# Performance work log

Hardware: AMD Instinct MI355X
Metric: run time of the kernel (lower is better)

## Reference

```python
import jax, jax.numpy as jnp
import numpy as np

EPS = 1e-5
H, I, E = 1024, 2048, 8


def _swiglu(x, wg, wu, wd):
    # x: [T,H], wg/wu: [H,I], wd: [I,H]
    return (jax.nn.silu(x @ wg) * (x @ wu)) @ wd


def setup_inputs() -> dict:
    key = jax.random.key(0)
    ks = jax.random.split(key, 12)
    B, S = 2, 2048
    s_h = 1.0 / np.sqrt(H)
    s_i = 1.0 / np.sqrt(I)
    return {
        "x": jax.random.normal(ks[0], (B, S, H), jnp.float32),
        "temporal_context": jax.random.normal(ks[1], (B, S, H), jnp.float32),
        "tp_w": jax.random.normal(ks[2], (H, H), jnp.float32) * s_h,
        "tp_b": jnp.zeros((H,), jnp.float32),
        "gate_w": jax.random.normal(ks[3], (H, E), jnp.float32) * 0.01,
        "eg": jax.random.normal(ks[4], (E, H, I), jnp.float32) * s_h,
        "eu": jax.random.normal(ks[5], (E, H, I), jnp.float32) * s_h,
        "ed": jax.random.normal(ks[6], (E, I, H), jnp.float32) * s_i,
        "sg": jax.random.normal(ks[7], (H, I), jnp.float32) * s_h,
        "su": jax.random.normal(ks[8], (H, I), jnp.float32) * s_h,
        "sd": jax.random.normal(ks[9], (I, H), jnp.float32) * s_i,
        "top_k": 2,
    }


def reference(x, temporal_context, tp_w, tp_b, gate_w, eg, eu, ed, sg, su, sd, top_k):
    B, S, Hd = x.shape
    xf = x.reshape(-1, Hd)                      # [T,H] tokens
    tc = temporal_context.reshape(-1, Hd)
    # Router: add temporal projection, softmax gate, top-k renormalized
    xr = xf + tc @ tp_w + tp_b
    probs = jax.nn.softmax(xr @ gate_w, axis=-1)            # [T,E]
    topk_p, topk_i = jax.lax.top_k(probs, top_k)            # [T,K]
    topk_p = topk_p / (topk_p.sum(-1, keepdims=True) + EPS)
    # Dense combine weights: combine[t,e] = sum_k topk_p[t,k] * 1[topk_i[t,k]==e]
    combine = jnp.einsum("tke,tk->te", jax.nn.one_hot(topk_i, E, dtype=x.dtype), topk_p)
    # Expert SwiGLU (grouped GEMM over all experts)
    h = jax.nn.silu(jnp.einsum("th,ehi->tei", xf, eg)) * jnp.einsum("th,ehi->tei", xf, eu)
    eout = jnp.einsum("tei,eih->teh", h, ed)                # [T,E,H]
    out = jnp.einsum("te,teh->th", combine, eout)
    # Shared expert applied to every token
    out = out + _swiglu(xf, sg, su, sd)
    return out.reshape(B, S, Hd)
```

## Files before the change

kernel.cpp:

```cpp
#include <hip/hip_runtime.h>
#include <hip/hip_bf16.h>
#include <stdint.h>

#define HDIM 1024
#define IDIM 2048
#define NEXP 8
#define NEXP1 9
#define TTOK 4096
#define REPS 1e-5f

typedef __bf16 bf16_t;
typedef __bf16 bf16x8 __attribute__((ext_vector_type(8)));
typedef __bf16 bf16x4 __attribute__((ext_vector_type(4)));
typedef float f32x4 __attribute__((ext_vector_type(4)));

__device__ __forceinline__ void gl_lds16(const bf16_t* g, bf16_t* l) {
    __builtin_amdgcn_global_load_lds(
        (const __attribute__((address_space(1))) void*)g,
        (__attribute__((address_space(3))) void*)l, 16, 0, 0);
}

__global__ __launch_bounds__(256) void k_convert(const float* __restrict__ src,
                                                 bf16_t* __restrict__ dst) {
    size_t i = ((size_t)blockIdx.x * 256 + threadIdx.x) * 4;
    float4 v = *(const float4*)(src + i);
    bf16x4 o = {(__bf16)v.x, (__bf16)v.y, (__bf16)v.z, (__bf16)v.w};
    *(bf16x4*)(dst + i) = o;
}

__global__ __launch_bounds__(256) void k_tr(const float* __restrict__ src,
                                            bf16_t* __restrict__ dst, int R, int C) {
    __shared__ __align__(16) bf16_t lds[128 * 64];
    size_t mat = (size_t)blockIdx.z * (size_t)R * (size_t)C;
    int c0 = blockIdx.x * 64, r0 = blockIdx.y * 128;
    int tid = threadIdx.x;

    int rlo = tid >> 4, chunk = tid & 15;
    for (int p = 0; p < 8; p++) {
        int r = p * 16 + rlo;
        float4 v = *(const float4*)(src + mat + (size_t)(r0 + r) * C + c0 + chunk * 4);
        bf16x4 o = {(__bf16)v.x, (__bf16)v.y, (__bf16)v.z, (__bf16)v.w};
        *(bf16x4*)(lds + r * 64 + ((chunk ^ p) & 15 ? ((chunk ^ (p & 7)) * 4) : ((chunk ^ (p & 7)) * 4))) = o;
    }
    __syncthreads();

    int c2 = tid & 31, rh = tid >> 5;
    uint32_t d[16];
    for (int i = 0; i < 16; i++) {
        int r = rh * 16 + i;
        d[i] = *(const uint32_t*)(lds + r * 64 + ((c2 >> 1) ^ (rh & 7)) * 4 + (c2 & 1) * 2);
    }
    uint32_t o0[8], o1[8];
    for (int j = 0; j < 8; j++) {
        uint32_t a = d[2 * j], b = d[2 * j + 1];
        o0[j] = (a & 0xffffu) | (b << 16);
        o1[j] = (a >> 16) | (b & 0xffff0000u);
    }
    bf16_t* p0 = dst + mat + (size_t)(c0 + 2 * c2) * R + r0 + rh * 16;
    bf16_t* p1 = p0 + R;
    *(uint4*)p0 = *(uint4*)&o0[0];
    *(uint4*)(p0 + 8) = *(uint4*)&o0[4];
    *(uint4*)p1 = *(uint4*)&o1[0];
    *(uint4*)(p1 + 8) = *(uint4*)&o1[4];
}

__global__ __launch_bounds__(256) void k_router_prep(const float* __restrict__ tp_w,
                                                     const float* __restrict__ tp_b,
                                                     const float* __restrict__ gw,
                                                     float* __restrict__ A_r,
                                                     float* __restrict__ bg) {
    int idx = blockIdx.x * 256 + threadIdx.x;
    if (idx < HDIM * NEXP) {
        int h = idx >> 3, e = idx & 7;
        const float* wr = tp_w + (size_t)h * HDIM;
        float acc = 0.f;
        for (int j = 0; j < HDIM; j++) acc = fmaf(wr[j], gw[j * NEXP + e], acc);
        A_r[idx] = acc;
    } else if (idx < HDIM * NEXP + NEXP) {
        int e = idx - HDIM * NEXP;
        float acc = 0.f;
        for (int j = 0; j < HDIM; j++) acc = fmaf(tp_b[j], gw[j * NEXP + e], acc);
        bg[e] = acc;
    }
}

__global__ __launch_bounds__(256) void k_router(const float* __restrict__ x,
                                                const float* __restrict__ tcx,
                                                const float* __restrict__ gw,
                                                const float* __restrict__ A_r,
                                                const float* __restrict__ bg,
                                                int* __restrict__ cnt, int* __restrict__ tok,
                                                float* __restrict__ wl, int* __restrict__ sl) {
    int wave = threadIdx.x >> 6, lane = threadIdx.x & 63;
    int t = blockIdx.x * 4 + wave;
    const float* xr = x + (size_t)t * HDIM;
    const float* tr = tcx + (size_t)t * HDIM;
    float lg[NEXP];
    for (int e = 0; e < NEXP; e++) lg[e] = 0.f;
    for (int h = lane; h < HDIM; h += 64) {
        float xv = xr[h], tv = tr[h];
        const float4* g4 = (const float4*)(gw + h * NEXP);
        const float4* a4 = (const float4*)(A_r + h * NEXP);
        float4 g0 = g4[0], g1 = g4[1], a0 = a4[0], a1 = a4[1];
        lg[0] += xv * g0.x + tv * a0.x;
        lg[1] += xv * g0.y + tv * a0.y;
        lg[2] += xv * g0.z + tv * a0.z;
        lg[3] += xv * g0.w + tv * a0.w;
        lg[4] += xv * g1.x + tv * a1.x;
        lg[5] += xv * g1.y + tv * a1.y;
        lg[6] += xv * g1.z + tv * a1.z;
        lg[7] += xv * g1.w + tv * a1.w;
    }
    for (int off = 32; off > 0; off >>= 1)
        for (int e = 0; e < NEXP; e++) lg[e] += __shfl_xor(lg[e], off);
    if (lane == 0) {
        float m = -1e30f;
        for (int e = 0; e < NEXP; e++) {
            lg[e] += bg[e];
            m = fmaxf(m, lg[e]);
        }
        float p[NEXP], Z = 0.f;
        for (int e = 0; e < NEXP; e++) {
            p[e] = __expf(lg[e] - m);
            Z += p[e];
        }
        for (int e = 0; e < NEXP; e++) p[e] /= Z;
        int i1 = 0;
        float b1 = p[0];
        for (int e = 1; e < NEXP; e++)
            if (p[e] > b1) { b1 = p[e]; i1 = e; }
        int i2 = -1;
        float b2 = -1.f;
        for (int e = 0; e < NEXP; e++) {
            if (e == i1) continue;
            if (p[e] > b2) { b2 = p[e]; i2 = e; }
        }
        float s = b1 + b2 + REPS;
        float w1 = b1 / s, w2 = b2 / s;
        int p1 = atomicAdd(&cnt[i1], 1);
        tok[i1 * TTOK + p1] = t;
        wl[i1 * TTOK + p1] = w1;
        sl[i1 * TTOK + p1] = 2 * t;
        int p2 = atomicAdd(&cnt[i2], 1);
        tok[i2 * TTOK + p2] = t;
        wl[i2 * TTOK + p2] = w2;
        sl[i2 * TTOK + p2] = 2 * t + 1;
    }
}

__global__ __launch_bounds__(256) void k_fill_shared(int* __restrict__ cnt, int* __restrict__ tok,
                                                     float* __restrict__ wl, int* __restrict__ sl) {
    int t = blockIdx.x * 256 + threadIdx.x;
    tok[NEXP * TTOK + t] = t;
    wl[NEXP * TTOK + t] = 1.f;
    sl[NEXP * TTOK + t] = 2 * TTOK + t;
    if (t == 0) cnt[NEXP] = TTOK;
}

__global__ __launch_bounds__(256, 2) void k_gateup(const bf16_t* __restrict__ Xb,
                                                   const bf16_t* __restrict__ WgT,
                                                   const bf16_t* __restrict__ WuT,
                                                   bf16_t* __restrict__ Hout,
                                                   const int* __restrict__ tok_l,
                                                   const float* __restrict__ w_l,
                                                   const int* __restrict__ slot_l,
                                                   const int* __restrict__ cnt) {
    int e = blockIdx.z;
    int rows = cnt[e];
    int m0 = blockIdx.y * 128;
    if (m0 >= rows) return;
    int n0 = blockIdx.x * 64;
    const bf16_t* Wg = WgT + (size_t)e * IDIM * HDIM;
    const bf16_t* Wu = WuT + (size_t)e * IDIM * HDIM;
    const int* tl = tok_l + e * TTOK;
    const float* wlp = w_l + e * TTOK;
    const int* sl = slot_l + e * TTOK;

    __shared__ __align__(16) bf16_t As[128 * 64];
    __shared__ __align__(16) bf16_t Bg[64 * 64];
    __shared__ __align__(16) bf16_t Bu[64 * 64];

    int tid = threadIdx.x;
    int lane = tid & 63, wave = tid >> 6;
    int lrow = lane >> 3;
    int lchunk = (lane & 7) ^ lrow;

    const bf16_t* asrc[4];
    for (int j = 0; j < 4; j++) {
        int r = (wave * 4 + j) * 8 + lrow;
        int row = tl[min(m0 + r, rows - 1)];
        asrc[j] = Xb + (size_t)row * HDIM + lchunk * 8;
    }
    const bf16_t* gsrc[2];
    const bf16_t* usrc[2];
    for (int j = 0; j < 2; j++) {
        int r = (wave * 2 + j) * 8 + lrow;
        gsrc[j] = Wg + (size_t)(n0 + r) * HDIM + lchunk * 8;
        usrc[j] = Wu + (size_t)(n0 + r) * HDIM + lchunk * 8;
    }

    f32x4 accg[2][4], accu[2][4];
    for (int a = 0; a < 2; a++)
        for (int b = 0; b < 4; b++) {
            accg[a][b] = (f32x4){0.f, 0.f, 0.f, 0.f};
            accu[a][b] = (f32x4){0.f, 0.f, 0.f, 0.f};
        }
    int lm = lane & 15, quad = lane >> 4, x7 = lm & 7;

    for (int k0 = 0; k0 < HDIM; k0 += 64) {
        for (int j = 0; j < 4; j++) gl_lds16(asrc[j] + k0, As + (wave * 4 + j) * 512);
        for (int j = 0; j < 2; j++) {
            gl_lds16(gsrc[j] + k0, Bg + (wave * 2 + j) * 512);
            gl_lds16(usrc[j] + k0, Bu + (wave * 2 + j) * 512);
        }
        __syncthreads();
        for (int kk = 0; kk < 2; kk++) {
            int cg = ((kk * 4 + quad) ^ x7) * 8;
            bf16x8 af[2], bgf[4], buf_[4];
            for (int mi = 0; mi < 2; mi++)
                af[mi] = *(const bf16x8*)&As[(wave * 32 + mi * 16 + lm) * 64 + cg];
            for (int ni = 0; ni < 4; ni++) {
                bgf[ni] = *(const bf16x8*)&Bg[(ni * 16 + lm) * 64 + cg];
                buf_[ni] = *(const bf16x8*)&Bu[(ni * 16 + lm) * 64 + cg];
            }
            for (int mi = 0; mi < 2; mi++)
                for (int ni = 0; ni < 4; ni++) {
                    accg[mi][ni] = __builtin_amdgcn_mfma_f32_16x16x32_bf16(af[mi], bgf[ni],
                                                                           accg[mi][ni], 0, 0, 0);
                    accu[mi][ni] = __builtin_amdgcn_mfma_f32_16x16x32_bf16(af[mi], buf_[ni],
                                                                           accu[mi][ni], 0, 0, 0);
                }
        }
        __syncthreads();
    }
    for (int mi = 0; mi < 2; mi++)
        for (int j = 0; j < 4; j++) {
            int r = m0 + wave * 32 + mi * 16 + quad * 4 + j;
            if (r >= rows) continue;
            int srow = sl[r];
            float w = wlp[r];
            bf16_t* hp = Hout + (size_t)srow * IDIM + n0 + lm;
            for (int ni = 0; ni < 4; ni++) {
                float g = accg[mi][ni][j];
                float u = accu[mi][ni][j];
                hp[ni * 16] = (bf16_t)(g / (1.f + __expf(-g)) * u * w);
            }
        }
}

__global__ __launch_bounds__(256, 2) void k_down(const bf16_t* __restrict__ Hin,
                                                 const bf16_t* __restrict__ WdT,
                                                 bf16_t* __restrict__ Eout,
                                                 const int* __restrict__ slot_l,
                                                 const int* __restrict__ cnt) {
    int e = blockIdx.z;
    int rows = cnt[e];
    int m0 = blockIdx.y * 128;
    if (m0 >= rows) return;
    int n0 = blockIdx.x * 128;
    const bf16_t* Wd = WdT + (size_t)e * HDIM * IDIM;
    const int* sl = slot_l + e * TTOK;

    __shared__ __align__(16) bf16_t As[128 * 64];
    __shared__ __align__(16) bf16_t Bs[128 * 64];

    int tid = threadIdx.x, lane = tid & 63, wave = tid >> 6;
    int lrow = lane >> 3;
    int lchunk = (lane & 7) ^ lrow;

    const bf16_t* asrc[4];
    const bf16_t* bsrc[4];
    for (int j = 0; j < 4; j++) {
        int r = (wave * 4 + j) * 8 + lrow;
        int arow = sl[min(m0 + r, rows - 1)];
        asrc[j] = Hin + (size_t)arow * IDIM + lchunk * 8;
        bsrc[j] = Wd + (size_t)(n0 + r) * IDIM + lchunk * 8;
    }
    f32x4 acc[4][4];
    for (int a = 0; a < 4; a++)
        for (int b = 0; b < 4; b++) acc[a][b] = (f32x4){0.f, 0.f, 0.f, 0.f};
    int wm = wave >> 1, wn = wave & 1;
    int lm = lane & 15, quad = lane >> 4, x7 = lm & 7;

    for (int k0 = 0; k0 < IDIM; k0 += 64) {
        for (int j = 0; j < 4; j++) {
            gl_lds16(asrc[j] + k0, As + (wave * 4 + j) * 512);
            gl_lds16(bsrc[j] + k0, Bs + (wave * 4 + j) * 512);
        }
        __syncthreads();
        for (int kk = 0; kk < 2; kk++) {
            int cg = ((kk * 4 + quad) ^ x7) * 8;
            bf16x8 af[4], bf_[4];
            for (int mi = 0; mi < 4; mi++)
                af[mi] = *(const bf16x8*)&As[(wm * 64 + mi * 16 + lm) * 64 + cg];
            for (int ni = 0; ni < 4; ni++)
                bf_[ni] = *(const bf16x8*)&Bs[(wn * 64 + ni * 16 + lm) * 64 + cg];
            for (int mi = 0; mi < 4; mi++)
                for (int ni = 0; ni < 4; ni++)
                    acc[mi][ni] = __builtin_amdgcn_mfma_f32_16x16x32_bf16(af[mi], bf_[ni],
                                                                          acc[mi][ni], 0, 0, 0);
        }
        __syncthreads();
    }
    for (int mi = 0; mi < 4; mi++)
        for (int j = 0; j < 4; j++) {
            int r = m0 + wm * 64 + mi * 16 + quad * 4 + j;
            if (r >= rows) continue;
            int srow = sl[r];
            bf16_t* op = Eout + (size_t)srow * HDIM + n0 + wn * 64 + lm;
            for (int ni = 0; ni < 4; ni++) op[ni * 16] = (bf16_t)acc[mi][ni][j];
        }
}

__global__ __launch_bounds__(256) void k_combine(const bf16_t* __restrict__ Eout,
                                                 float* __restrict__ Out) {
    size_t i = ((size_t)blockIdx.x * 256 + threadIdx.x) * 8;
    size_t t = i / HDIM, h = i % HDIM;
    bf16x8 a = *(const bf16x8*)(Eout + (2 * t) * HDIM + h);
    bf16x8 b = *(const bf16x8*)(Eout + (2 * t + 1) * HDIM + h);
    bf16x8 c = *(const bf16x8*)(Eout + (size_t)(2 * TTOK + t) * HDIM + h);
    float* op = Out + i;
    for (int j = 0; j < 8; j++) op[j] = (float)a[j] + (float)b[j] + (float)c[j];
}

extern "C" void kernel_launch(void* const* d_in, const int* in_sizes, int n_in,
                              void* d_out, int out_size, void* d_ws, size_t ws_size,
                              hipStream_t stream) {
    const float* x = (const float*)d_in[0];
    const float* tcx = (const float*)d_in[1];
    const float* tp_w = (const float*)d_in[2];
    const float* tp_b = (const float*)d_in[3];
    const float* gate_w = (const float*)d_in[4];
    const float* eg = (const float*)d_in[5];
    const float* eu = (const float*)d_in[6];
    const float* ed = (const float*)d_in[7];
    const float* sg = (const float*)d_in[8];
    const float* su = (const float*)d_in[9];
    const float* sd = (const float*)d_in[10];
    float* out = (float*)d_out;

    char* wsp = (char*)d_ws;
    size_t off = 0;
    auto alloc = [&](size_t b) -> void* {
        void* p = wsp + off;
        off += (b + 255) & ~(size_t)255;
        return p;
    };
    bf16_t* xb = (bf16_t*)alloc((size_t)TTOK * HDIM * 2);
    bf16_t* WgT = (bf16_t*)alloc((size_t)NEXP1 * IDIM * HDIM * 2);
    bf16_t* WuT = (bf16_t*)alloc((size_t)NEXP1 * IDIM * HDIM * 2);
    bf16_t* WdT = (bf16_t*)alloc((size_t)NEXP1 * HDIM * IDIM * 2);
    float* A_r = (float*)alloc(HDIM * NEXP * 4);
    float* bg = (float*)alloc(NEXP * 4);
    int* cnt = (int*)alloc(NEXP1 * 4);
    int* tok = (int*)alloc(NEXP1 * TTOK * 4);
    float* wl = (float*)alloc(NEXP1 * TTOK * 4);
    int* sl = (int*)alloc(NEXP1 * TTOK * 4);
    bf16_t* hbuf = (bf16_t*)alloc((size_t)3 * TTOK * IDIM * 2);
    bf16_t* eout = (bf16_t*)alloc((size_t)3 * TTOK * HDIM * 2);

    hipMemsetAsync(cnt, 0, NEXP1 * 4, stream);
    k_convert<<<TTOK * HDIM / 1024, 256, 0, stream>>>(x, xb);
    k_tr<<<dim3(IDIM / 64, HDIM / 128, NEXP), 256, 0, stream>>>(eg, WgT, HDIM, IDIM);
    k_tr<<<dim3(IDIM / 64, HDIM / 128, NEXP), 256, 0, stream>>>(eu, WuT, HDIM, IDIM);
    k_tr<<<dim3(IDIM / 64, HDIM / 128, 1), 256, 0, stream>>>(
        sg, WgT + (size_t)NEXP * IDIM * HDIM, HDIM, IDIM);
    k_tr<<<dim3(IDIM / 64, HDIM / 128, 1), 256, 0, stream>>>(
        su, WuT + (size_t)NEXP * IDIM * HDIM, HDIM, IDIM);
    k_tr<<<dim3(HDIM / 64, IDIM / 128, NEXP), 256, 0, stream>>>(ed, WdT, IDIM, HDIM);
    k_tr<<<dim3(HDIM / 64, IDIM / 128, 1), 256, 0, stream>>>(
        sd, WdT + (size_t)NEXP * HDIM * IDIM, IDIM, HDIM);
    k_router_prep<<<33, 256, 0, stream>>>(tp_w, tp_b, gate_w, A_r, bg);
    k_router<<<TTOK / 4, 256, 0, stream>>>(x, tcx, gate_w, A_r, bg, cnt, tok, wl, sl);
    k_fill_shared<<<TTOK / 256, 256, 0, stream>>>(cnt, tok, wl, sl);
    k_gateup<<<dim3(IDIM / 64, TTOK / 128, NEXP1), 256, 0, stream>>>(xb, WgT, WuT, hbuf, tok, wl,
                                                                     sl, cnt);
    k_down<<<dim3(HDIM / 128, TTOK / 128, NEXP1), 256, 0, stream>>>(hbuf, WdT, eout, sl, cnt);
    k_combine<<<TTOK * HDIM / 2048, 256, 0, stream>>>(eout, out);
    (void)in_sizes; (void)n_in; (void)out_size; (void)ws_size;
}
```

Before: 646.5 us.

## Widen gate/up GEMM tile to 128x128 and merge transpose/fill launches

```diff
diff --git a/kernel.cpp b/kernel.cpp
--- a/kernel.cpp
+++ b/kernel.cpp
@@ -28,22 +28,17 @@
     *(bf16x4*)(dst + i) = o;
 }
 
-__global__ __launch_bounds__(256) void k_tr(const float* __restrict__ src,
-                                            bf16_t* __restrict__ dst, int R, int C) {
-    __shared__ __align__(16) bf16_t lds[128 * 64];
-    size_t mat = (size_t)blockIdx.z * (size_t)R * (size_t)C;
-    int c0 = blockIdx.x * 64, r0 = blockIdx.y * 128;
+__device__ __forceinline__ void tr_tile(const float* __restrict__ src, bf16_t* __restrict__ dst,
+                                        int R, int C, int c0, int r0, bf16_t* lds) {
     int tid = threadIdx.x;
-
     int rlo = tid >> 4, chunk = tid & 15;
     for (int p = 0; p < 8; p++) {
         int r = p * 16 + rlo;
-        float4 v = *(const float4*)(src + mat + (size_t)(r0 + r) * C + c0 + chunk * 4);
+        float4 v = *(const float4*)(src + (size_t)(r0 + r) * C + c0 + chunk * 4);
         bf16x4 o = {(__bf16)v.x, (__bf16)v.y, (__bf16)v.z, (__bf16)v.w};
-        *(bf16x4*)(lds + r * 64 + ((chunk ^ p) & 15 ? ((chunk ^ (p & 7)) * 4) : ((chunk ^ (p & 7)) * 4))) = o;
+        *(bf16x4*)(lds + r * 64 + (chunk ^ (p & 7)) * 4) = o;
     }
     __syncthreads();
-
     int c2 = tid & 31, rh = tid >> 5;
     uint32_t d[16];
     for (int i = 0; i < 16; i++) {
@@ -56,12 +51,41 @@
         o0[j] = (a & 0xffffu) | (b << 16);
         o1[j] = (a >> 16) | (b & 0xffff0000u);
     }
-    bf16_t* p0 = dst + mat + (size_t)(c0 + 2 * c2) * R + r0 + rh * 16;
+    bf16_t* p0 = dst + (size_t)(c0 + 2 * c2) * R + r0 + rh * 16;
     bf16_t* p1 = p0 + R;
     *(uint4*)p0 = *(uint4*)&o0[0];
     *(uint4*)(p0 + 8) = *(uint4*)&o0[4];
     *(uint4*)p1 = *(uint4*)&o1[0];
     *(uint4*)(p1 + 8) = *(uint4*)&o1[4];
+}
+
+__global__ __launch_bounds__(256) void k_tr_HI(const float* __restrict__ eg,
+                                               const float* __restrict__ eu,
+                                               const float* __restrict__ sg,
+                                               const float* __restrict__ su,
+                                               bf16_t* __restrict__ WgT,
+                                               bf16_t* __restrict__ WuT) {
+    __shared__ __align__(16) bf16_t lds[128 * 64];
+    int z = blockIdx.z;
+    const float* src;
+    bf16_t* dst;
+    size_t msz = (size_t)HDIM * IDIM;
+    if (z < 8)       { src = eg + z * msz;        dst = WgT + z * msz; }
+    else if (z < 16) { src = eu + (z - 8) * msz;  dst = WuT + (z - 8) * msz; }
+    else if (z == 16){ src = sg;                  dst = WgT + 8 * msz; }
+    else             { src = su;                  dst = WuT + 8 * msz; }
+    tr_tile(src, dst, HDIM, IDIM, blockIdx.x * 64, blockIdx.y * 128, lds);
+}
+
+__global__ __launch_bounds__(256) void k_tr_IH(const float* __restrict__ ed,
+                                               const float* __restrict__ sd,
+                                               bf16_t* __restrict__ WdT) {
+    __shared__ __align__(16) bf16_t lds[128 * 64];
+    int z = blockIdx.z;
+    size_t msz = (size_t)HDIM * IDIM;
+    const float* src = (z < 8) ? ed + z * msz : sd;
+    bf16_t* dst = WdT + ((z < 8) ? z : 8) * msz;
+    tr_tile(src, dst, IDIM, HDIM, blockIdx.x * 64, blockIdx.y * 128, lds);
 }
 
 __global__ __launch_bounds__(256) void k_router_prep(const float* __restrict__ tp_w,
@@ -113,6 +137,12 @@
     }
     for (int off = 32; off > 0; off >>= 1)
         for (int e = 0; e < NEXP; e++) lg[e] += __shfl_xor(lg[e], off);
+    if (lane == 1) {
+        tok[NEXP * TTOK + t] = t;
+        wl[NEXP * TTOK + t] = 1.f;
+        sl[NEXP * TTOK + t] = 2 * TTOK + t;
+        if (t == 0) cnt[NEXP] = TTOK;
+    }
     if (lane == 0) {
         float m = -1e30f;
         for (int e = 0; e < NEXP; e++) {
@@ -146,15 +176,6 @@
         wl[i2 * TTOK + p2] = w2;
         sl[i2 * TTOK + p2] = 2 * t + 1;
     }
-}
-
-__global__ __launch_bounds__(256) void k_fill_shared(int* __restrict__ cnt, int* __restrict__ tok,
-                                                     float* __restrict__ wl, int* __restrict__ sl) {
-    int t = blockIdx.x * 256 + threadIdx.x;
-    tok[NEXP * TTOK + t] = t;
-    wl[NEXP * TTOK + t] = 1.f;
-    sl[NEXP * TTOK + t] = 2 * TTOK + t;
-    if (t == 0) cnt[NEXP] = TTOK;
 }
 
 __global__ __launch_bounds__(256, 2) void k_gateup(const bf16_t* __restrict__ Xb,
@@ -169,7 +190,7 @@
     int rows = cnt[e];
     int m0 = blockIdx.y * 128;
     if (m0 >= rows) return;
-    int n0 = blockIdx.x * 64;
+    int n0 = blockIdx.x * 128;
     const bf16_t* Wg = WgT + (size_t)e * IDIM * HDIM;
     const bf16_t* Wu = WuT + (size_t)e * IDIM * HDIM;
     const int* tl = tok_l + e * TTOK;
@@ -177,8 +198,8 @@
     const int* sl = slot_l + e * TTOK;
 
     __shared__ __align__(16) bf16_t As[128 * 64];
-    __shared__ __align__(16) bf16_t Bg[64 * 64];
-    __shared__ __align__(16) bf16_t Bu[64 * 64];
+    __shared__ __align__(16) bf16_t Bg[128 * 64];
+    __shared__ __align__(16) bf16_t Bu[128 * 64];
 
     int tid = threadIdx.x;
     int lane = tid & 63, wave = tid >> 6;
@@ -186,44 +207,42 @@
     int lchunk = (lane & 7) ^ lrow;
 
     const bf16_t* asrc[4];
+    const bf16_t* gsrc[4];
+    const bf16_t* usrc[4];
     for (int j = 0; j < 4; j++) {
         int r = (wave * 4 + j) * 8 + lrow;
-        int row = tl[min(m0 + r, rows - 1)];
-        asrc[j] = Xb + (size_t)row * HDIM + lchunk * 8;
-    }
-    const bf16_t* gsrc[2];
-    const bf16_t* usrc[2];
-    for (int j = 0; j < 2; j++) {
-        int r = (wave * 2 + j) * 8 + lrow;
+        int arow = tl[min(m0 + r, rows - 1)];
+        asrc[j] = Xb + (size_t)arow * HDIM + lchunk * 8;
         gsrc[j] = Wg + (size_t)(n0 + r) * HDIM + lchunk * 8;
         usrc[j] = Wu + (size_t)(n0 + r) * HDIM + lchunk * 8;
     }
 
-    f32x4 accg[2][4], accu[2][4];
-    for (int a = 0; a < 2; a++)
+    f32x4 accg[4][4], accu[4][4];
+    for (int a = 0; a < 4; a++)
         for (int b = 0; b < 4; b++) {
             accg[a][b] = (f32x4){0.f, 0.f, 0.f, 0.f};
             accu[a][b] = (f32x4){0.f, 0.f, 0.f, 0.f};
         }
+    int wm = wave >> 1, wn = wave & 1;
     int lm = lane & 15, quad = lane >> 4, x7 = lm & 7;
 
     for (int k0 = 0; k0 < HDIM; k0 += 64) {
-        for (int j = 0; j < 4; j++) gl_lds16(asrc[j] + k0, As + (wave * 4 + j) * 512);
-        for (int j = 0; j < 2; j++) {
-            gl_lds16(gsrc[j] + k0, Bg + (wave * 2 + j) * 512);
-            gl_lds16(usrc[j] + k0, Bu + (wave * 2 + j) * 512);
+        for (int j = 0; j < 4; j++) {
+            gl_lds16(asrc[j] + k0, As + (wave * 4 + j) * 512);
+            gl_lds16(gsrc[j] + k0, Bg + (wave * 4 + j) * 512);
+            gl_lds16(usrc[j] + k0, Bu + (wave * 4 + j) * 512);
         }
         __syncthreads();
         for (int kk = 0; kk < 2; kk++) {
             int cg = ((kk * 4 + quad) ^ x7) * 8;
-            bf16x8 af[2], bgf[4], buf_[4];
-            for (int mi = 0; mi < 2; mi++)
-                af[mi] = *(const bf16x8*)&As[(wave * 32 + mi * 16 + lm) * 64 + cg];
+            bf16x8 af[4], bgf[4], buf_[4];
+            for (int mi = 0; mi < 4; mi++)
+                af[mi] = *(const bf16x8*)&As[(wm * 64 + mi * 16 + lm) * 64 + cg];
             for (int ni = 0; ni < 4; ni++) {
-                bgf[ni] = *(const bf16x8*)&Bg[(ni * 16 + lm) * 64 + cg];
-                buf_[ni] = *(const bf16x8*)&Bu[(ni * 16 + lm) * 64 + cg];
+                bgf[ni] = *(const bf16x8*)&Bg[(wn * 64 + ni * 16 + lm) * 64 + cg];
+                buf_[ni] = *(const bf16x8*)&Bu[(wn * 64 + ni * 16 + lm) * 64 + cg];
             }
-            for (int mi = 0; mi < 2; mi++)
+            for (int mi = 0; mi < 4; mi++)
                 for (int ni = 0; ni < 4; ni++) {
                     accg[mi][ni] = __builtin_amdgcn_mfma_f32_16x16x32_bf16(af[mi], bgf[ni],
                                                                            accg[mi][ni], 0, 0, 0);
@@ -233,13 +252,13 @@
         }
         __syncthreads();
     }
-    for (int mi = 0; mi < 2; mi++)
+    for (int mi = 0; mi < 4; mi++)
         for (int j = 0; j < 4; j++) {
-            int r = m0 + wave * 32 + mi * 16 + quad * 4 + j;
+            int r = m0 + wm * 64 + mi * 16 + quad * 4 + j;
             if (r >= rows) continue;
             int srow = sl[r];
             float w = wlp[r];
-            bf16_t* hp = Hout + (size_t)srow * IDIM + n0 + lm;
+            bf16_t* hp = Hout + (size_t)srow * IDIM + n0 + wn * 64 + lm;
             for (int ni = 0; ni < 4; ni++) {
                 float g = accg[mi][ni][j];
                 float u = accu[mi][ni][j];
@@ -361,20 +380,12 @@
 
     hipMemsetAsync(cnt, 0, NEXP1 * 4, stream);
     k_convert<<<TTOK * HDIM / 1024, 256, 0, stream>>>(x, xb);
-    k_tr<<<dim3(IDIM / 64, HDIM / 128, NEXP), 256, 0, stream>>>(eg, WgT, HDIM, IDIM);
-    k_tr<<<dim3(IDIM / 64, HDIM / 128, NEXP), 256, 0, stream>>>(eu, WuT, HDIM, IDIM);
-    k_tr<<<dim3(IDIM / 64, HDIM / 128, 1), 256, 0, stream>>>(
-        sg, WgT + (size_t)NEXP * IDIM * HDIM, HDIM, IDIM);
-    k_tr<<<dim3(IDIM / 64, HDIM / 128, 1), 256, 0, stream>>>(
-        su, WuT + (size_t)NEXP * IDIM * HDIM, HDIM, IDIM);
-    k_tr<<<dim3(HDIM / 64, IDIM / 128, NEXP), 256, 0, stream>>>(ed, WdT, IDIM, HDIM);
-    k_tr<<<dim3(HDIM / 64, IDIM / 128, 1), 256, 0, stream>>>(
-        sd, WdT + (size_t)NEXP * HDIM * IDIM, IDIM, HDIM);
+    k_tr_HI<<<dim3(IDIM / 64, HDIM / 128, 18), 256, 0, stream>>>(eg, eu, sg, su, WgT, WuT);
+    k_tr_IH<<<dim3(HDIM / 64, IDIM / 128, 9), 256, 0, stream>>>(ed, sd, WdT);
     k_router_prep<<<33, 256, 0, stream>>>(tp_w, tp_b, gate_w, A_r, bg);
     k_router<<<TTOK / 4, 256, 0, stream>>>(x, tcx, gate_w, A_r, bg, cnt, tok, wl, sl);
-    k_fill_shared<<<TTOK / 256, 256, 0, stream>>>(cnt, tok, wl, sl);
-    k_gateup<<<dim3(IDIM / 64, TTOK / 128, NEXP1), 256, 0, stream>>>(xb, WgT, WuT, hbuf, tok, wl,
-                                                                     sl, cnt);
+    k_gateup<<<dim3(IDIM / 128, TTOK / 128, NEXP1), 256, 0, stream>>>(xb, WgT, WuT, hbuf, tok, wl,
+                                                                      sl, cnt);
     k_down<<<dim3(HDIM / 128, TTOK / 128, NEXP1), 256, 0, stream>>>(hbuf, WdT, eout, sl, cnt);
     k_combine<<<TTOK * HDIM / 2048, 256, 0, stream>>>(eout, out);
     (void)in_sizes; (void)n_in; (void)out_size; (void)ws_size;
```

After: 655.4 us. No clear change (+1.4%).
